# Kernel tuning notes

Hardware: AMD Instinct MI355X
Metric: run time of the kernel (lower is better)

The kernel has to match this reference:

```python
import jax, jax.numpy as jnp
import numpy as np

B, S, E, H, L, DFF = 2, 2048, 512, 8, 2, 2048
D = E // H
EPS = 1e-5


def layernorm(x, g, b):
    mu = jnp.mean(x, axis=-1, keepdims=True)
    var = jnp.var(x, axis=-1, keepdims=True)
    return (x - mu) * jax.lax.rsqrt(var + EPS) * g + b


def layernorm_noaffine(x):
    mu = jnp.mean(x, axis=-1, keepdims=True)
    var = jnp.var(x, axis=-1, keepdims=True)
    return (x - mu) * jax.lax.rsqrt(var + EPS)


def setup_inputs() -> dict:
    key = jax.random.key(0)
    ks = jax.random.split(key, 16)
    s = 0.02
    inp = {
        "x": jax.random.normal(ks[0], (B, S, E), dtype=jnp.float32),
        "mask": jax.random.randint(ks[1], (B, S), 0, 2) == 1,
        # per-layer attention projections, stacked over layers
        "wq": jax.random.normal(ks[2], (L, E, E), dtype=jnp.float32) * s,
        "bq": jnp.zeros((L, E), dtype=jnp.float32),
        "wk": jax.random.normal(ks[3], (L, E, E), dtype=jnp.float32) * s,
        "bk": jnp.zeros((L, E), dtype=jnp.float32),
        "wv": jax.random.normal(ks[4], (L, E, E), dtype=jnp.float32) * s,
        "bv": jnp.zeros((L, E), dtype=jnp.float32),
        # shared norms (module defines a single norm1/norm2 used by every layer)
        "g1": jnp.ones((E,), dtype=jnp.float32),
        "b1": jnp.zeros((E,), dtype=jnp.float32),
        "g2": jnp.ones((E,), dtype=jnp.float32),
        "b2": jnp.zeros((E,), dtype=jnp.float32),
        "gf": jnp.ones((E,), dtype=jnp.float32),
        "bf": jnp.zeros((E,), dtype=jnp.float32),
        # shared Dense FFN (single self.dense used after every layer)
        "W1": jax.random.normal(ks[5], (DFF, E), dtype=jnp.float32) * s,
        "B1": jnp.zeros((DFF,), dtype=jnp.float32),
        "W2": jax.random.normal(ks[6], (E, DFF), dtype=jnp.float32) * s,
        "B2": jnp.zeros((E,), dtype=jnp.float32),
    }
    return inp


def _forward(x, wq, bq, wk, bk, wv, bv, g1, b1, g2, b2, gf, bf, W1, B1, W2, B2, mask):
    scale = 1.0 / jnp.sqrt(jnp.float32(D))
    m = mask[:, None, None, :]  # [B,1,1,S] key padding mask, True = pad
    neg_inf = jnp.float32(-jnp.inf)
    for i in range(L):
        h = layernorm(x, g1, b1)  # norm1(x), used for q,k,v
        q = (h @ wq[i].T + bq[i]).reshape(B, S, H, D).transpose(0, 2, 1, 3)
        k = (h @ wk[i].T + bk[i]).reshape(B, S, H, D).transpose(0, 2, 1, 3)
        v = (h @ wv[i].T + bv[i]).reshape(B, S, H, D).transpose(0, 2, 1, 3)
        logits = jnp.einsum("bhqd,bhkd->bhqk", q, k) * scale
        att = jax.nn.softmax(jnp.where(m, neg_inf, logits), axis=-1)
        att = jnp.where(m, 0.0, att)
        out = jnp.einsum("bhqk,bhkd->bhqd", att, v)
        out = out.transpose(0, 2, 1, 3).reshape(B, S, E)
        x = x + layernorm(out, g2, b2)
        # Dense: LayerNorm(no affine) -> Linear -> ReLU -> Linear, residual
        d = layernorm_noaffine(x)
        d = jax.nn.relu(d @ W1.T + B1)
        d = d @ W2.T + B2
        x = x + d
    return layernorm(x, gf, bf)


def reference(x, mask, wq, bq, wk, bk, wv, bv, g1, b1, g2, b2, gf, bf, W1, B1, W2, B2):
    return _forward(x, wq, bq, wk, bk, wv, bv, g1, b1, g2, b2, gf, bf, W1, B1, W2, B2, mask)
```

## Files before the change

### kernel.cpp

```cpp
#include <hip/hip_runtime.h>
#include <hip/hip_bf16.h>

constexpr int BB   = 2;
constexpr int SS   = 2048;
constexpr int EE   = 512;
constexpr int HH   = 8;
constexpr int DD   = 64;
constexpr int DFF_ = 2048;
constexpr int NTOK = BB * SS;
constexpr int NE   = NTOK * EE;
constexpr float EPSF  = 1e-5f;
constexpr float SCL2  = 0.125f * 1.44269504088896f;
constexpr float MBIAS = -1e30f;
constexpr int KSPLIT = 2;
constexpr int KHALF  = SS / KSPLIT;

typedef __bf16 v8bf __attribute__((ext_vector_type(8)));
typedef __bf16 v4bf __attribute__((ext_vector_type(4)));
typedef float  v4f  __attribute__((ext_vector_type(4)));

__device__ __forceinline__ float bf2f(unsigned short u) {
    return __uint_as_float(((unsigned int)u) << 16);
}
__device__ __forceinline__ float bf2f(__bf16 u) {
    unsigned short us = __builtin_bit_cast(unsigned short, u);
    return __uint_as_float(((unsigned int)us) << 16);
}
__device__ __forceinline__ float ldA(const void* p, size_t i, int f) {
    return f ? ((const float*)p)[i] : bf2f(((const unsigned short*)p)[i]);
}
__device__ __forceinline__ void gll16(const void* g, void* l) {
    __builtin_amdgcn_global_load_lds(
        (const __attribute__((address_space(1))) void*)g,
        (__attribute__((address_space(3))) void*)l, 16, 0, 0);
}

__global__ void sniff_kernel(const unsigned short* __restrict__ x, int* flag) {
    __shared__ int cnt[256];
    int t = threadIdx.x, bad = 0;
    for (int i = t; i < 4096; i += 256) {
        float v = bf2f(x[i]);
        if (!(fabsf(v) < 1000.f)) bad++;
    }
    cnt[t] = bad;
    __syncthreads();
    if (t == 0) {
        int s = 0;
        for (int i = 0; i < 256; ++i) s += cnt[i];
        *flag = (s > 8) ? 1 : 0;
    }
}

__global__ __launch_bounds__(256) void cvt_ln(
    const void* __restrict__ in, float* __restrict__ X,
    const void* __restrict__ g, const void* __restrict__ b,
    __bf16* __restrict__ Hb, const int* __restrict__ flagp)
{
    const int f = *flagp;
    const int row = blockIdx.x, t = threadIdx.x;
    const size_t i0 = (size_t)row * EE + t, i1 = i0 + 256;
    float v0 = ldA(in, i0, f);
    float v1 = ldA(in, i1, f);
    float s = v0 + v1, q = v0 * v0 + v1 * v1;
    #pragma unroll
    for (int off = 32; off > 0; off >>= 1) {
        s += __shfl_down(s, off, 64);
        q += __shfl_down(q, off, 64);
    }
    __shared__ float red[8], st[2];
    const int wid = t >> 6;
    if ((t & 63) == 0) { red[wid] = s; red[4 + wid] = q; }
    __syncthreads();
    if (t == 0) {
        float S_ = red[0] + red[1] + red[2] + red[3];
        float Q_ = red[4] + red[5] + red[6] + red[7];
        float mu = S_ / EE;
        st[0] = mu;
        st[1] = rsqrtf(Q_ / EE - mu * mu + EPSF);
    }
    __syncthreads();
    const float mu = st[0], rs = st[1];
    float o0 = (v0 - mu) * rs * ldA(g, t, f)       + ldA(b, t, f);
    float o1 = (v1 - mu) * rs * ldA(g, t + 256, f) + ldA(b, t + 256, f);
    X[i0] = v0; X[i1] = v1;
    Hb[i0] = (__bf16)o0; Hb[i1] = (__bf16)o1;
}

__global__ void wcvt_all(const void* __restrict__ wq, const void* __restrict__ wk,
                         const void* __restrict__ wv, const void* __restrict__ W1,
                         const void* __restrict__ W2, __bf16* __restrict__ out,
                         const int* __restrict__ flagp) {
    const int f = *flagp;
    const int i = (blockIdx.x * blockDim.x + threadIdx.x) * 8;
    constexpr int n1 = 2 * EE * EE;
    constexpr int nf = DFF_ * EE;
    const void* src; int off;
    if      (i < n1)          { src = wq; off = i; }
    else if (i < 2 * n1)      { src = wk; off = i - n1; }
    else if (i < 3 * n1)      { src = wv; off = i - 2 * n1; }
    else if (i < 3 * n1 + nf) { src = W1; off = i - 3 * n1; }
    else                      { src = W2; off = i - 3 * n1 - nf; }
    if (f) {
        const float* p = (const float*)src + off;
        #pragma unroll
        for (int j = 0; j < 8; ++j) out[i + j] = (__bf16)p[j];
    } else {
        *(uint4*)(out + i) = *(const uint4*)((const unsigned short*)src + off);
    }
}

__global__ __launch_bounds__(256) void ln_kernel(
    const float* __restrict__ src,
    const void* __restrict__ g, const void* __restrict__ b,
    __bf16* __restrict__ dstb, void* __restrict__ outp,
    const int* __restrict__ flagp)
{
    const int f = *flagp;
    const int row = blockIdx.x, t = threadIdx.x;
    const float* x = src + (size_t)row * EE;
    float v0 = x[t], v1 = x[t + 256];
    float s = v0 + v1, q = v0 * v0 + v1 * v1;
    #pragma unroll
    for (int off = 32; off > 0; off >>= 1) {
        s += __shfl_down(s, off, 64);
        q += __shfl_down(q, off, 64);
    }
    __shared__ float red[8], st[2];
    const int wid = t >> 6;
    if ((t & 63) == 0) { red[wid] = s; red[4 + wid] = q; }
    __syncthreads();
    if (t == 0) {
        float S_ = red[0] + red[1] + red[2] + red[3];
        float Q_ = red[4] + red[5] + red[6] + red[7];
        float mu = S_ / EE;
        st[0] = mu;
        st[1] = rsqrtf(Q_ / EE - mu * mu + EPSF);
    }
    __syncthreads();
    const float mu = st[0], rs = st[1];
    float o0 = (v0 - mu) * rs, o1 = (v1 - mu) * rs;
    if (g) {
        o0 = o0 * ldA(g, t, f)       + ldA(b, t, f);
        o1 = o1 * ldA(g, t + 256, f) + ldA(b, t + 256, f);
    }
    const size_t i0 = (size_t)row * EE + t, i1 = i0 + 256;
    if (dstb) { dstb[i0] = (__bf16)o0; dstb[i1] = (__bf16)o1; }
    if (outp) {
        if (f) { ((float*)outp)[i0] = o0; ((float*)outp)[i1] = o1; }
        else {
            ((__hip_bfloat16*)outp)[i0] = __float2bfloat16(o0);
            ((__hip_bfloat16*)outp)[i1] = __float2bfloat16(o1);
        }
    }
}

__global__ __launch_bounds__(256) void combine_ln(
    const __bf16* __restrict__ Opart, const float* __restrict__ MLl,
    const void* __restrict__ g2, const void* __restrict__ b2,
    float* __restrict__ X, __bf16* __restrict__ Hb,
    const int* __restrict__ flagp)
{
    const int f = *flagp;
    const int tok = blockIdx.x, t = threadIdx.x;
    const int b = tok >> 11, s_ = tok & 2047;
    __shared__ float cinv[8];
    __shared__ float red[8], st[2];
    if (t < 8) {
        float l = 0.f;
        #pragma unroll
        for (int zz = 0; zz < KSPLIT; ++zz)
            l += MLl[(size_t)(zz * 16 + b * 8 + t) * SS + s_];
        cinv[t] = (l > 0.f) ? 1.f / l : 0.f;
    }
    __syncthreads();
    float a0 = 0.f, a1 = 0.f;
    {
        int c = t, h = c >> 6, d = c & 63;
        #pragma unroll
        for (int zz = 0; zz < KSPLIT; ++zz)
            a0 += bf2f(Opart[((size_t)(zz * 16 + b * 8 + h) * SS + s_) * 64 + d]);
        a0 *= cinv[h];
        c = t + 256; h = c >> 6; d = c & 63;
        #pragma unroll
        for (int zz = 0; zz < KSPLIT; ++zz)
            a1 += bf2f(Opart[((size_t)(zz * 16 + b * 8 + h) * SS + s_) * 64 + d]);
        a1 *= cinv[h];
    }
    const int wid = t >> 6;
    {
        float s = a0 + a1, q = a0 * a0 + a1 * a1;
        #pragma unroll
        for (int off = 32; off > 0; off >>= 1) {
            s += __shfl_down(s, off, 64);
            q += __shfl_down(q, off, 64);
        }
        if ((t & 63) == 0) { red[wid] = s; red[4 + wid] = q; }
    }
    __syncthreads();
    if (t == 0) {
        float S_ = red[0] + red[1] + red[2] + red[3];
        float Q_ = red[4] + red[5] + red[6] + red[7];
        float mu = S_ / EE;
        st[0] = mu;
        st[1] = rsqrtf(Q_ / EE - mu * mu + EPSF);
    }
    __syncthreads();
    const float mu1 = st[0], rs1 = st[1];
    const size_t i0 = (size_t)tok * EE + t, i1 = i0 + 256;
    float l0v = (a0 - mu1) * rs1 * ldA(g2, t, f)       + ldA(b2, t, f);
    float l1v = (a1 - mu1) * rs1 * ldA(g2, t + 256, f) + ldA(b2, t + 256, f);
    float x0 = X[i0] + l0v, x1 = X[i1] + l1v;
    __syncthreads();
    {
        float s = x0 + x1, q = x0 * x0 + x1 * x1;
        #pragma unroll
        for (int off = 32; off > 0; off >>= 1) {
            s += __shfl_down(s, off, 64);
            q += __shfl_down(q, off, 64);
        }
        if ((t & 63) == 0) { red[wid] = s; red[4 + wid] = q; }
    }
    __syncthreads();
    if (t == 0) {
        float S_ = red[0] + red[1] + red[2] + red[3];
        float Q_ = red[4] + red[5] + red[6] + red[7];
        float mu = S_ / EE;
        st[0] = mu;
        st[1] = rsqrtf(Q_ / EE - mu * mu + EPSF);
    }
    __syncthreads();
    const float mu2 = st[0], rs2 = st[1];
    X[i0] = x0; X[i1] = x1;
    Hb[i0] = (__bf16)((x0 - mu2) * rs2);
    Hb[i1] = (__bf16)((x1 - mu2) * rs2);
}

__global__ __launch_bounds__(256) void gemm_mfma(
    const __bf16* __restrict__ A,
    const __bf16* Wa, const __bf16* Wb, const __bf16* Wc,
    const void* ba, const void* bb, const void* bc,
    __bf16* oa, __bf16* ob, __bf16* oc,
    float* __restrict__ Cf,
    int M, int N, int K, int flags,
    size_t welem_off, size_t belem_off, const int* __restrict__ flagp)
{
    const int f = *flagp;
    const int z = blockIdx.z;
    const __bf16* W = (z == 0) ? Wa : (z == 1) ? Wb : Wc;
    const void* bias = (z == 0) ? ba : (z == 1) ? bb : bc;
    __bf16* Cb = (z == 0) ? oa : (z == 1) ? ob : oc;
    W += welem_off;
    int kbeg = 0, kend = K;
    if (flags & 4) {
        const int ks = K >> 2;
        kbeg = z * ks; kend = kbeg + ks;
        if (z != 0) bias = nullptr;
    }

    __shared__ __bf16 As[2][128 * 64];
    __shared__ __bf16 Bs[2][128 * 64];
    const int t = threadIdx.x;
    const int w = t >> 6, lane = t & 63;
    const int quad = lane >> 4, l16 = lane & 15;
    const int wr = w >> 1, wc = w & 1;
    const int bm = blockIdx.x * 128, bn = blockIdx.y * 128;

    v4f acc[4][4] = {};

    #define STAGE_TILE(dst, src, rowbase, kk)                                   \
        _Pragma("unroll")                                                       \
        for (int ii = 0; ii < 4; ++ii) {                                        \
            const int c  = t + 256 * ii;                                        \
            const int r  = c >> 3, cc = c & 7;                                  \
            const int es = ((cc ^ (r & 7)) * 8);                                \
            gll16(src + (size_t)(rowbase + r) * K + kk + es,                    \
                  (char*)(dst) + c * 16);                                       \
        }

    STAGE_TILE(As[0], A, bm, kbeg)
    STAGE_TILE(Bs[0], W, bn, kbeg)

    int p = 0;
    for (int k0 = kbeg; k0 < kend; k0 += 64) {
        __syncthreads();
        if (k0 + 64 < kend) {
            const int kn = k0 + 64, q_ = p ^ 1;
            STAGE_TILE(As[q_], A, bm, kn)
            STAGE_TILE(Bs[q_], W, bn, kn)
        }
        #pragma unroll
        for (int ks = 0; ks < 2; ++ks) {
            v8bf af[4], bfr[4];
            #pragma unroll
            for (int i = 0; i < 4; ++i) {
                const int row = wr * 64 + i * 16 + l16;
                const int ph  = (quad + ks * 4) ^ (row & 7);
                af[i] = *(const v8bf*)&As[p][row * 64 + ph * 8];
            }
            #pragma unroll
            for (int j = 0; j < 4; ++j) {
                const int row = wc * 64 + j * 16 + l16;
                const int ph  = (quad + ks * 4) ^ (row & 7);
                bfr[j] = *(const v8bf*)&Bs[p][row * 64 + ph * 8];
            }
            #pragma unroll
            for (int i = 0; i < 4; ++i)
                #pragma unroll
                for (int j = 0; j < 4; ++j)
                    acc[i][j] = __builtin_amdgcn_mfma_f32_16x16x32_bf16(
                        af[i], bfr[j], acc[i][j], 0, 0, 0);
        }
        p ^= 1;
    }
    #undef STAGE_TILE

    float bvv[4];
    #pragma unroll
    for (int j = 0; j < 4; ++j) {
        int col = bn + wc * 64 + j * 16 + l16;
        bvv[j] = bias ? ldA(bias, belem_off + col, f) : 0.f;
    }

    if ((flags & 8) && z == 2) {
        #pragma unroll
        for (int i = 0; i < 4; ++i) {
            const int row0 = bm + wr * 64 + i * 16 + quad * 4;
            const int b_ = row0 >> 11, sl = row0 & 2047;
            const int s64 = sl & ~63, sloc = sl & 63;
            const int slot = (sloc & 32) + ((sloc >> 2) & 3) * 8 + ((sloc >> 4) & 1) * 4;
            #pragma unroll
            for (int j = 0; j < 4; ++j) {
                const int col = bn + wc * 64 + j * 16 + l16;
                const int h_ = col >> 6, d_ = col & 63;
                v4bf u;
                #pragma unroll
                for (int r = 0; r < 4; ++r) u[r] = (__bf16)(acc[i][j][r] + bvv[j]);
                *(v4bf*)(Cb + ((size_t)((b_ * 8 + h_) * 64 + d_)) * SS + s64 + slot) = u;
            }
        }
        return;
    }

    #pragma unroll
    for (int i = 0; i < 4; ++i) {
        const int rowb = bm + wr * 64 + i * 16 + quad * 4;
        #pragma unroll
        for (int j = 0; j < 4; ++j) {
            const int col = bn + wc * 64 + j * 16 + l16;
            #pragma unroll
            for (int r = 0; r < 4; ++r) {
                float v = acc[i][j][r] + bvv[j];
                if (flags & 1) v = fmaxf(v, 0.f);
                const size_t idx = (size_t)(rowb + r) * N + col;
                if (flags & 4)      unsafeAtomicAdd(&Cf[idx], v);
                else if (flags & 2) Cf[idx] += v;
                else                Cb[idx] = (__bf16)v;
            }
        }
    }
}

__global__ __launch_bounds__(256) void attn_mfma(
    const __bf16* __restrict__ Qg, const __bf16* __restrict__ Kg,
    const __bf16* __restrict__ Vtg, const int* __restrict__ mask,
    __bf16* __restrict__ Opart, float* __restrict__ MLl)
{
    __shared__ __bf16 Ks[64][72];
    __shared__ __bf16 Vs[64][72];
    __shared__ float  mkf[64];

    const int t = threadIdx.x;
    const int w = t >> 6, lane = t & 63;
    const int quad = lane >> 4, l16 = lane & 15;
    const int bh = blockIdx.y, b = bh >> 3, hh = bh & 7;
    const int q0 = blockIdx.x * 128;
    const int z  = blockIdx.z;
    const int kof = z * KHALF;

    const __bf16* qrow0 = Qg + ((size_t)(b * SS + q0 + w * 32 + l16)) * EE + hh * DD + quad * 8;
    const __bf16* qrow1 = qrow0 + (size_t)16 * EE;
    const v8bf qa00 = *(const v8bf*)qrow0;
    const v8bf qa01 = *(const v8bf*)(qrow0 + 32);
    const v8bf qa10 = *(const v8bf*)qrow1;
    const v8bf qa11 = *(const v8bf*)(qrow1 + 32);

    const int lr = t >> 2, lc = (t & 3) * 16;
    const __bf16* kbase = Kg  + ((size_t)(b * SS + kof + lr)) * EE + hh * DD + lc;
    const __bf16* vbase = Vtg + ((size_t)((b * 8 + hh) * 64 + lr)) * SS + kof + lc;

    v8bf ka0 = *(const v8bf*)kbase, ka1 = *(const v8bf*)(kbase + 8);
    v8bf va0 = *(const v8bf*)vbase, va1 = *(const v8bf*)(vbase + 8);
    float mb = 0.f;
    if (t < 64) mb = mask[b * SS + kof + t] ? MBIAS : 0.f;

    float l0 = 0.f, l1 = 0.f;
    v4f o0[4] = {}, o1[4] = {};

    #pragma unroll 1
    for (int k0 = 0; k0 < KHALF; k0 += 64) {
        *(v8bf*)&Ks[lr][lc]     = ka0;
        *(v8bf*)&Ks[lr][lc + 8] = ka1;
        *(v8bf*)&Vs[lr][lc]     = va0;
        *(v8bf*)&Vs[lr][lc + 8] = va1;
        if (t < 64) mkf[t] = mb;
        __syncthreads();
        if (k0 + 64 < KHALF) {
            ka0 = *(const v8bf*)(kbase + (size_t)(k0 + 64) * EE);
            ka1 = *(const v8bf*)(kbase + (size_t)(k0 + 64) * EE + 8);
            va0 = *(const v8bf*)(vbase + (k0 + 64));
            va1 = *(const v8bf*)(vbase + (k0 + 64) + 8);
            if (t < 64) mb = mask[b * SS + kof + k0 + 64 + t] ? MBIAS : 0.f;
        }

        v4f s0[4], s1[4];
        __builtin_amdgcn_s_setprio(1);
        #pragma unroll
        for (int j = 0; j < 4; ++j) {
            v8bf kf0 = *(const v8bf*)&Ks[j * 16 + l16][quad * 8];
            v8bf kf1 = *(const v8bf*)&Ks[j * 16 + l16][32 + quad * 8];
            v4f za = {}, zb = {};
            za = __builtin_amdgcn_mfma_f32_16x16x32_bf16(kf0, qa00, za, 0, 0, 0);
            za = __builtin_amdgcn_mfma_f32_16x16x32_bf16(kf1, qa01, za, 0, 0, 0);
            zb = __builtin_amdgcn_mfma_f32_16x16x32_bf16(kf0, qa10, zb, 0, 0, 0);
            zb = __builtin_amdgcn_mfma_f32_16x16x32_bf16(kf1, qa11, zb, 0, 0, 0);
            s0[j] = za; s1[j] = zb;
        }
        __builtin_amdgcn_s_setprio(0);
        float4 mk4[4];
        #pragma unroll
        for (int j = 0; j < 4; ++j) mk4[j] = *(const float4*)&mkf[j * 16 + quad * 4];

        v8bf p00, p01, p10, p11;
        float t0 = 0.f, t1 = 0.f;
        #pragma unroll
        for (int j = 0; j < 4; ++j) {
            float a0 = exp2f(fmaf(s0[j][0], SCL2, mk4[j].x));
            float a1 = exp2f(fmaf(s0[j][1], SCL2, mk4[j].y));
            float a2 = exp2f(fmaf(s0[j][2], SCL2, mk4[j].z));
            float a3 = exp2f(fmaf(s0[j][3], SCL2, mk4[j].w));
            float b0 = exp2f(fmaf(s1[j][0], SCL2, mk4[j].x));
            float b1 = exp2f(fmaf(s1[j][1], SCL2, mk4[j].y));
            float b2 = exp2f(fmaf(s1[j][2], SCL2, mk4[j].z));
            float b3 = exp2f(fmaf(s1[j][3], SCL2, mk4[j].w));
            t0 += (a0 + a1) + (a2 + a3);
            t1 += (b0 + b1) + (b2 + b3);
            if (j < 2) {
                p00[j * 4 + 0] = (__bf16)a0; p00[j * 4 + 1] = (__bf16)a1;
                p00[j * 4 + 2] = (__bf16)a2; p00[j * 4 + 3] = (__bf16)a3;
                p10[j * 4 + 0] = (__bf16)b0; p10[j * 4 + 1] = (__bf16)b1;
                p10[j * 4 + 2] = (__bf16)b2; p10[j * 4 + 3] = (__bf16)b3;
            } else {
                p01[(j - 2) * 4 + 0] = (__bf16)a0; p01[(j - 2) * 4 + 1] = (__bf16)a1;
                p01[(j - 2) * 4 + 2] = (__bf16)a2; p01[(j - 2) * 4 + 3] = (__bf16)a3;
                p11[(j - 2) * 4 + 0] = (__bf16)b0; p11[(j - 2) * 4 + 1] = (__bf16)b1;
                p11[(j - 2) * 4 + 2] = (__bf16)b2; p11[(j - 2) * 4 + 3] = (__bf16)b3;
            }
        }
        l0 += t0; l1 += t1;

        __builtin_amdgcn_s_setprio(1);
        #pragma unroll
        for (int dt = 0; dt < 4; ++dt) {
            v8bf vf0 = *(const v8bf*)&Vs[dt * 16 + l16][quad * 8];
            v8bf vf1 = *(const v8bf*)&Vs[dt * 16 + l16][32 + quad * 8];
            o0[dt] = __builtin_amdgcn_mfma_f32_16x16x32_bf16(vf0, p00, o0[dt], 0, 0, 0);
            o0[dt] = __builtin_amdgcn_mfma_f32_16x16x32_bf16(vf1, p01, o0[dt], 0, 0, 0);
            o1[dt] = __builtin_amdgcn_mfma_f32_16x16x32_bf16(vf0, p10, o1[dt], 0, 0, 0);
            o1[dt] = __builtin_amdgcn_mfma_f32_16x16x32_bf16(vf1, p11, o1[dt], 0, 0, 0);
        }
        __builtin_amdgcn_s_setprio(0);
        __syncthreads();
    }

    l0 += __shfl_xor(l0, 16, 64);
    l0 += __shfl_xor(l0, 32, 64);
    l1 += __shfl_xor(l1, 16, 64);
    l1 += __shfl_xor(l1, 32, 64);

    const size_t qi0 = (size_t)(z * 16 + bh) * SS + (q0 + w * 32 + l16);
    const size_t qi1 = qi0 + 16;
    __bf16* op0 = Opart + qi0 * 64;
    __bf16* op1 = Opart + qi1 * 64;
    #pragma unroll
    for (int dt = 0; dt < 4; ++dt) {
        v4bf u0, u1;
        #pragma unroll
        for (int r = 0; r < 4; ++r) { u0[r] = (__bf16)o0[dt][r]; u1[r] = (__bf16)o1[dt][r]; }
        *(v4bf*)(op0 + dt * 16 + quad * 4) = u0;
        *(v4bf*)(op1 + dt * 16 + quad * 4) = u1;
    }
    if (quad == 0) { MLl[qi0] = l0; MLl[qi1] = l1; }
}

extern "C" void kernel_launch(void* const* d_in, const int* in_sizes, int n_in,
                              void* d_out, int out_size, void* d_ws, size_t ws_size,
                              hipStream_t stream) {
    const void* x_in = d_in[0];
    const int*  mask = (const int*)d_in[1];
    const void* wq = d_in[2];  const void* bq = d_in[3];
    const void* wk = d_in[4];  const void* bk = d_in[5];
    const void* wv = d_in[6];  const void* bv = d_in[7];
    const void* g1 = d_in[8];  const void* b1 = d_in[9];
    const void* g2 = d_in[10]; const void* b2 = d_in[11];
    const void* gf = d_in[12]; const void* bfp= d_in[13];
    const void* W1 = d_in[14]; const void* B1 = d_in[15];
    const void* W2 = d_in[16]; const void* B2 = d_in[17];

    float* base = (float*)d_ws;
    int*   flag = (int*)base;
    float* X   = base + 16;
    float* fQ  = X + NE;
    float* fK  = fQ + NE / 2;
    float* fV  = fK + NE / 2;
    float* fH  = fV + NE / 2;
    float* fW  = fH + NE / 2;
    __bf16* Qb    = (__bf16*)fQ;
    __bf16* Kb    = (__bf16*)fK;
    __bf16* Vtg   = (__bf16*)fV;
    __bf16* Hb    = (__bf16*)fH;
    __bf16* wqc = (__bf16*)fW;
    __bf16* wkc = wqc + 2 * EE * EE;
    __bf16* wvc = wkc + 2 * EE * EE;
    __bf16* W1c = wvc + 2 * EE * EE;
    __bf16* W2c = W1c + DFF_ * EE;
    float* MLl = (float*)(W2c + (size_t)EE * DFF_);
    float* fO  = MLl + (size_t)KSPLIT * 16 * SS;
    __bf16* Opart = (__bf16*)fO;
    __bf16* MID   = (__bf16*)fO;

    sniff_kernel<<<1, 256, 0, stream>>>((const unsigned short*)x_in, flag);
    cvt_ln<<<NTOK, 256, 0, stream>>>(x_in, X, g1, b1, Hb, flag);
    wcvt_all<<<1792, 256, 0, stream>>>(wq, wk, wv, W1, W2, wqc, flag);

    const dim3 gQKV(NTOK / 128, EE / 128, 3);
    const dim3 gF1 (NTOK / 128, DFF_ / 128, 1);
    const dim3 gF2 (NTOK / 128, EE / 128, 4);
    const dim3 gAtt(SS / 128, BB * HH, KSPLIT);

    for (int l = 0; l < 2; ++l) {
        const size_t wo = (size_t)l * EE * EE, bo = (size_t)l * EE;
        if (l > 0)
            ln_kernel<<<NTOK, 256, 0, stream>>>(X, g1, b1, Hb, nullptr, flag);
        gemm_mfma<<<gQKV, 256, 0, stream>>>(Hb, wqc, wkc, wvc, bq, bk, bv,
            Qb, Kb, Vtg, nullptr, NTOK, EE, EE, 8, wo, bo, flag);
        attn_mfma<<<gAtt, 256, 0, stream>>>(Qb, Kb, Vtg, mask, Opart, MLl);
        combine_ln<<<NTOK, 256, 0, stream>>>(Opart, MLl, g2, b2, X, Hb, flag);
        gemm_mfma<<<gF1, 256, 0, stream>>>(Hb, W1c, W1c, W1c, B1, B1, B1,
            MID, MID, MID, nullptr, NTOK, DFF_, EE, 1, 0, 0, flag);
        gemm_mfma<<<gF2, 256, 0, stream>>>(MID, W2c, W2c, W2c, B2, B2, B2,
            nullptr, nullptr, nullptr, X, NTOK, EE, DFF_, 2 | 4, 0, 0, flag);
    }
    ln_kernel<<<NTOK, 256, 0, stream>>>(X, gf, bfp, nullptr, d_out, flag);
}
```

Baseline: 358.9 us.

## Add dedicated 128x64-tile QKV GEMM and fold dtype sniff into first LN

Adds a specialized QKV projection GEMM with 128x64 tiles, so the grid doubles in the N dimension and more blocks fill the device for the small K=512 GEMM. It has its own XOR-swizzled LDS staging and the V-transpose epilogue, which is removed from the generic GEMM. The separate single-block dtype sniff kernel is removed, and every cvt_ln block now recomputes the flag from the first 512 elements, cutting one launch. The recomputed flag uses a smaller sample and a different threshold than before.

```diff
diff --git a/kernel.cpp b/kernel.cpp
--- a/kernel.cpp
+++ b/kernel.cpp
@@ -35,29 +35,32 @@
         (__attribute__((address_space(3))) void*)l, 16, 0, 0);
 }
 
-__global__ void sniff_kernel(const unsigned short* __restrict__ x, int* flag) {
-    __shared__ int cnt[256];
-    int t = threadIdx.x, bad = 0;
-    for (int i = t; i < 4096; i += 256) {
-        float v = bf2f(x[i]);
-        if (!(fabsf(v) < 1000.f)) bad++;
-    }
-    cnt[t] = bad;
-    __syncthreads();
-    if (t == 0) {
-        int s = 0;
-        for (int i = 0; i < 256; ++i) s += cnt[i];
-        *flag = (s > 8) ? 1 : 0;
-    }
-}
-
 __global__ __launch_bounds__(256) void cvt_ln(
     const void* __restrict__ in, float* __restrict__ X,
     const void* __restrict__ g, const void* __restrict__ b,
-    __bf16* __restrict__ Hb, const int* __restrict__ flagp)
+    __bf16* __restrict__ Hb, int* __restrict__ flagw)
 {
-    const int f = *flagp;
     const int row = blockIdx.x, t = threadIdx.x;
+    __shared__ float red[8], st[2];
+    __shared__ int scnt[4], sflag;
+    {
+        const unsigned short* u = (const unsigned short*)in;
+        int bad = 0;
+        #pragma unroll
+        for (int i = 0; i < 2; ++i) {
+            float v = bf2f(u[t + 256 * i]);
+            if (!(fabsf(v) < 1000.f)) bad++;
+        }
+        #pragma unroll
+        for (int off = 32; off > 0; off >>= 1) bad += __shfl_down(bad, off, 64);
+        if ((t & 63) == 0) scnt[t >> 6] = bad;
+        __syncthreads();
+        if (t == 0) sflag = (scnt[0] + scnt[1] + scnt[2] + scnt[3] > 1) ? 1 : 0;
+        __syncthreads();
+    }
+    const int f = sflag;
+    if (row == 0 && t == 0) *flagw = f;
+
     const size_t i0 = (size_t)row * EE + t, i1 = i0 + 256;
     float v0 = ldA(in, i0, f);
     float v1 = ldA(in, i1, f);
@@ -67,7 +70,6 @@
         s += __shfl_down(s, off, 64);
         q += __shfl_down(q, off, 64);
     }
-    __shared__ float red[8], st[2];
     const int wid = t >> 6;
     if ((t & 63) == 0) { red[wid] = s; red[4 + wid] = q; }
     __syncthreads();
@@ -321,26 +323,6 @@
         bvv[j] = bias ? ldA(bias, belem_off + col, f) : 0.f;
     }
 
-    if ((flags & 8) && z == 2) {
-        #pragma unroll
-        for (int i = 0; i < 4; ++i) {
-            const int row0 = bm + wr * 64 + i * 16 + quad * 4;
-            const int b_ = row0 >> 11, sl = row0 & 2047;
-            const int s64 = sl & ~63, sloc = sl & 63;
-            const int slot = (sloc & 32) + ((sloc >> 2) & 3) * 8 + ((sloc >> 4) & 1) * 4;
-            #pragma unroll
-            for (int j = 0; j < 4; ++j) {
-                const int col = bn + wc * 64 + j * 16 + l16;
-                const int h_ = col >> 6, d_ = col & 63;
-                v4bf u;
-                #pragma unroll
-                for (int r = 0; r < 4; ++r) u[r] = (__bf16)(acc[i][j][r] + bvv[j]);
-                *(v4bf*)(Cb + ((size_t)((b_ * 8 + h_) * 64 + d_)) * SS + s64 + slot) = u;
-            }
-        }
-        return;
-    }
-
     #pragma unroll
     for (int i = 0; i < 4; ++i) {
         const int rowb = bm + wr * 64 + i * 16 + quad * 4;
@@ -355,6 +337,127 @@
                 if (flags & 4)      unsafeAtomicAdd(&Cf[idx], v);
                 else if (flags & 2) Cf[idx] += v;
                 else                Cb[idx] = (__bf16)v;
+            }
+        }
+    }
+}
+
+__global__ __launch_bounds__(256) void gemm_qkv(
+    const __bf16* __restrict__ A,
+    const __bf16* Wa, const __bf16* Wb, const __bf16* Wc,
+    const void* ba, const void* bb, const void* bc,
+    __bf16* oa, __bf16* ob, __bf16* oc,
+    size_t welem_off, size_t belem_off, const int* __restrict__ flagp)
+{
+    const int f = *flagp;
+    const int z = blockIdx.z;
+    const __bf16* W = (z == 0) ? Wa : (z == 1) ? Wb : Wc;
+    const void* bias = (z == 0) ? ba : (z == 1) ? bb : bc;
+    __bf16* Cb = (z == 0) ? oa : (z == 1) ? ob : oc;
+    W += welem_off;
+    constexpr int K = EE, N = EE;
+
+    __shared__ __bf16 As[2][128 * 64];
+    __shared__ __bf16 Bs[2][64 * 64];
+    const int t = threadIdx.x;
+    const int w = t >> 6, lane = t & 63;
+    const int quad = lane >> 4, l16 = lane & 15;
+    const int bm = blockIdx.x * 128, bn = blockIdx.y * 64;
+
+    v4f acc[2][4] = {};
+
+    #define STAGE_A(dst, kk)                                                    \
+        _Pragma("unroll")                                                       \
+        for (int ii = 0; ii < 4; ++ii) {                                        \
+            const int c  = t + 256 * ii;                                        \
+            const int r  = c >> 3, cc = c & 7;                                  \
+            const int es = ((cc ^ (r & 7)) * 8);                                \
+            gll16(A + (size_t)(bm + r) * K + kk + es, (char*)(dst) + c * 16);   \
+        }
+    #define STAGE_B(dst, kk)                                                    \
+        _Pragma("unroll")                                                       \
+        for (int ii = 0; ii < 2; ++ii) {                                        \
+            const int c  = t + 256 * ii;                                        \
+            const int r  = c >> 3, cc = c & 7;                                  \
+            const int es = ((cc ^ (r & 7)) * 8);                                \
+            gll16(W + (size_t)(bn + r) * K + kk + es, (char*)(dst) + c * 16);   \
+        }
+
+    STAGE_A(As[0], 0)
+    STAGE_B(Bs[0], 0)
+
+    int p = 0;
+    for (int k0 = 0; k0 < K; k0 += 64) {
+        __syncthreads();
+        if (k0 + 64 < K) {
+            const int kn = k0 + 64, q_ = p ^ 1;
+            STAGE_A(As[q_], kn)
+            STAGE_B(Bs[q_], kn)
+        }
+        #pragma unroll
+        for (int ks = 0; ks < 2; ++ks) {
+            v8bf af[2], bfr[4];
+            #pragma unroll
+            for (int i = 0; i < 2; ++i) {
+                const int row = w * 32 + i * 16 + l16;
+                const int ph  = (quad + ks * 4) ^ (row & 7);
+                af[i] = *(const v8bf*)&As[p][row * 64 + ph * 8];
+            }
+            #pragma unroll
+            for (int j = 0; j < 4; ++j) {
+                const int row = j * 16 + l16;
+                const int ph  = (quad + ks * 4) ^ (row & 7);
+                bfr[j] = *(const v8bf*)&Bs[p][row * 64 + ph * 8];
+            }
+            #pragma unroll
+            for (int i = 0; i < 2; ++i)
+                #pragma unroll
+                for (int j = 0; j < 4; ++j)
+                    acc[i][j] = __builtin_amdgcn_mfma_f32_16x16x32_bf16(
+                        af[i], bfr[j], acc[i][j], 0, 0, 0);
+        }
+        p ^= 1;
+    }
+    #undef STAGE_A
+    #undef STAGE_B
+
+    float bvv[4];
+    #pragma unroll
+    for (int j = 0; j < 4; ++j) {
+        int col = bn + j * 16 + l16;
+        bvv[j] = bias ? ldA(bias, belem_off + col, f) : 0.f;
+    }
+
+    if (z == 2) {
+        #pragma unroll
+        for (int i = 0; i < 2; ++i) {
+            const int row0 = bm + w * 32 + i * 16 + quad * 4;
+            const int b_ = row0 >> 11, sl = row0 & 2047;
+            const int s64 = sl & ~63, sloc = sl & 63;
+            const int slot = (sloc & 32) + ((sloc >> 2) & 3) * 8 + ((sloc >> 4) & 1) * 4;
+            #pragma unroll
+            for (int j = 0; j < 4; ++j) {
+                const int col = bn + j * 16 + l16;
+                const int h_ = col >> 6, d_ = col & 63;
+                v4bf u;
+                #pragma unroll
+                for (int r = 0; r < 4; ++r) u[r] = (__bf16)(acc[i][j][r] + bvv[j]);
+                *(v4bf*)(Cb + ((size_t)((b_ * 8 + h_) * 64 + d_)) * SS + s64 + slot) = u;
+            }
+        }
+        return;
+    }
+
+    #pragma unroll
+    for (int i = 0; i < 2; ++i) {
+        const int rowb = bm + w * 32 + i * 16 + quad * 4;
+        #pragma unroll
+        for (int j = 0; j < 4; ++j) {
+            const int col = bn + j * 16 + l16;
+            #pragma unroll
+            for (int r = 0; r < 4; ++r) {
+                const size_t idx = (size_t)(rowb + r) * N + col;
+                Cb[idx] = (__bf16)(acc[i][j][r] + bvv[j]);
             }
         }
     }
@@ -528,11 +631,10 @@
     __bf16* Opart = (__bf16*)fO;
     __bf16* MID   = (__bf16*)fO;
 
-    sniff_kernel<<<1, 256, 0, stream>>>((const unsigned short*)x_in, flag);
     cvt_ln<<<NTOK, 256, 0, stream>>>(x_in, X, g1, b1, Hb, flag);
     wcvt_all<<<1792, 256, 0, stream>>>(wq, wk, wv, W1, W2, wqc, flag);
 
-    const dim3 gQKV(NTOK / 128, EE / 128, 3);
+    const dim3 gQKV(NTOK / 128, EE / 64, 3);
     const dim3 gF1 (NTOK / 128, DFF_ / 128, 1);
     const dim3 gF2 (NTOK / 128, EE / 128, 4);
     const dim3 gAtt(SS / 128, BB * HH, KSPLIT);
@@ -541,8 +643,8 @@
         const size_t wo = (size_t)l * EE * EE, bo = (size_t)l * EE;
         if (l > 0)
             ln_kernel<<<NTOK, 256, 0, stream>>>(X, g1, b1, Hb, nullptr, flag);
-        gemm_mfma<<<gQKV, 256, 0, stream>>>(Hb, wqc, wkc, wvc, bq, bk, bv,
-            Qb, Kb, Vtg, nullptr, NTOK, EE, EE, 8, wo, bo, flag);
+        gemm_qkv<<<gQKV, 256, 0, stream>>>(Hb, wqc, wkc, wvc, bq, bk, bv,
+            Qb, Kb, Vtg, wo, bo, flag);
         attn_mfma<<<gAtt, 256, 0, stream>>>(Qb, Kb, Vtg, mask, Opart, MLl);
         combine_ln<<<NTOK, 256, 0, stream>>>(Opart, MLl, g2, b2, X, Hb, flag);
         gemm_mfma<<<gF1, 256, 0, stream>>>(Hb, W1c, W1c, W1c, B1, B1, B1,
```

After: 350.7 us. 1.02x faster.
